# Optimization experiments

Measured on AMD Instinct MI355X. Metric: run time of the kernel, lower is better.

## Reference

```python
import jax, jax.numpy as jnp
import numpy as np

H = 16
D_MODEL = 1024
D_K = D_MODEL // H  # 64, must equal embeddim


def setup_inputs() -> dict:
    key = jax.random.key(0)
    ks = jax.random.split(key, 20)
    B, S, D = 4, 1024, D_MODEL
    s = 0.02
    inp = {
        'query': jax.random.normal(ks[0], (B, S, D), jnp.float32),
        'key':   jax.random.normal(ks[1], (B, S, D), jnp.float32),
        'value': jax.random.normal(ks[2], (B, S, D), jnp.float32),
        'mask':  jnp.ones((B, S, S), jnp.int32),
        # four d_model x d_model projections (q, k, v, out)
        'wq': jax.random.normal(ks[3], (D, D), jnp.float32) * s, 'bq': jnp.zeros((D,), jnp.float32),
        'wk': jax.random.normal(ks[4], (D, D), jnp.float32) * s, 'bk': jnp.zeros((D,), jnp.float32),
        'wv': jax.random.normal(ks[5], (D, D), jnp.float32) * s, 'bv': jnp.zeros((D,), jnp.float32),
        'wo': jax.random.normal(ks[6], (D, D), jnp.float32) * s, 'bo': jnp.zeros((D,), jnp.float32),
        # per-head (embeddim=64) linears
        'spatial_w': jax.random.normal(ks[7], (D_K, D_K), jnp.float32) * s, 'spatial_b': jnp.zeros((D_K,), jnp.float32),
        'qproj_w':   jax.random.normal(ks[8], (D_K, D_K), jnp.float32) * s, 'qproj_b':   jnp.zeros((D_K,), jnp.float32),
        'kproj_w':   jax.random.normal(ks[9], (D_K, D_K), jnp.float32) * s, 'kproj_b':   jnp.zeros((D_K,), jnp.float32),
        'vlin_w':    jax.random.normal(ks[10], (D_K, D_K), jnp.float32) * s, 'vlin_b':    jnp.zeros((D_K,), jnp.float32),
        # channel_linear: Linear(1, 64)
        'chan_w': jax.random.normal(ks[11], (1, D_K), jnp.float32) * s, 'chan_b': jnp.zeros((D_K,), jnp.float32),
    }
    return inp


def reference(query, key, value, mask,
              wq, bq, wk, bk, wv, bv, wo, bo,
              spatial_w, spatial_b, qproj_w, qproj_b,
              kproj_w, kproj_b, vlin_w, vlin_b, chan_w, chan_b):
    B, S, D = query.shape
    # project and split heads -> [B, H, S, D_K]
    def heads(x, w, b):
        return (x @ w + b).reshape(B, S, H, D_K).transpose(0, 2, 1, 3)
    q = heads(query, wq, bq)
    k = heads(key, wk, bk)
    v = heads(value, wv, bv)

    q = jax.nn.elu(q @ spatial_w + spatial_b)
    q_refine = q @ qproj_w + qproj_b
    # channel gate: mean over channels -> Linear(1,64) -> matmul with raw key
    alpha = q_refine.mean(-1, keepdims=True) @ chan_w + chan_b        # [B,H,S,64]
    gate = jax.nn.sigmoid(jnp.einsum('bhqe,bhke->bhqk', alpha, k))    # [B,H,S,S]

    k2 = jax.nn.elu(k @ kproj_w + kproj_b)
    scores = jnp.einsum('bhqe,bhke->bhqk', q, k2) / jnp.sqrt(jnp.asarray(D_K, q.dtype))
    scores = scores * gate
    scores = jnp.where(mask[:, None] == 0, jnp.asarray(-1e9, scores.dtype), scores)
    p_attn = jax.nn.softmax(scores, axis=-1)

    v2 = jax.nn.elu(v @ vlin_w + vlin_b)
    x = jnp.einsum('bhqk,bhke->bhqe', p_attn, v2)                     # [B,H,S,64]
    x = x.transpose(0, 2, 1, 3).reshape(B, S, H * D_K)
    return x @ wo + bo
```

## Files before the change

### kernel.cpp

```cpp
#include <hip/hip_runtime.h>
#include <math.h>

#define D_MODEL 1024
#define NH 16
#define DK 64
#define S_LEN 1024
#define BATCH 4
#define MROWS (BATCH * S_LEN)

typedef short bf16x8 __attribute__((ext_vector_type(8)));
typedef float f32x4 __attribute__((ext_vector_type(4)));
typedef unsigned short u16;

__device__ __forceinline__ float elu1(float x) {
    return x > 0.f ? x : (expf(x) - 1.f);
}

__device__ __forceinline__ u16 f2bf(float f) {
    union { float f; unsigned u; } v; v.f = f;
    unsigned u = v.u;
    return (u16)((u + 0x7fffu + ((u >> 16) & 1u)) >> 16);
}

__device__ __forceinline__ u16 f2bf_fast(float f) {
    union { float f; unsigned u; } v; v.f = f;
    return (u16)((v.u + 0x8000u) >> 16);
}

__device__ __forceinline__ void async16(const void* g, void* l) {
    __builtin_amdgcn_global_load_lds(
        (const __attribute__((address_space(1))) unsigned int*)g,
        (__attribute__((address_space(3))) unsigned int*)l,
        16, 0, 0);
}

__global__ __launch_bounds__(256) void prep(
    const float* __restrict__ wq, const float* __restrict__ wk,
    const float* __restrict__ wv, const float* __restrict__ wo,
    u16* __restrict__ WT,
    const float* __restrict__ Xq, const float* __restrict__ Xk,
    const float* __restrict__ Xv, u16* __restrict__ Xb,
    const int* __restrict__ mask, unsigned long long* __restrict__ Mb)
{
    __shared__ float T[64][65];
    const int bid = blockIdx.x;
    const int tid = threadIdx.x;

    if (bid < 1024) {
        const int z = bid >> 8;
        const int rem = bid & 255;
        const int n0 = (rem & 15) * 64, k0 = (rem >> 4) * 64;
        const float* W = (z == 0) ? wq : ((z == 1) ? wk : ((z == 2) ? wv : wo));
        u16* O = WT + (size_t)z * D_MODEL * D_MODEL;
        const int r = tid >> 4, c4 = (tid & 15) * 4;
        #pragma unroll
        for (int p = 0; p < 4; p++) {
            float4 v = *(const float4*)&W[(size_t)(k0 + r + p * 16) * D_MODEL + n0 + c4];
            T[r + p * 16][c4 + 0] = v.x; T[r + p * 16][c4 + 1] = v.y;
            T[r + p * 16][c4 + 2] = v.z; T[r + p * 16][c4 + 3] = v.w;
        }
        __syncthreads();
        #pragma unroll
        for (int p = 0; p < 4; p++) {
            const int i = r + p * 16;
            ushort4 o4;
            o4.x = f2bf(T[c4 + 0][i]); o4.y = f2bf(T[c4 + 1][i]);
            o4.z = f2bf(T[c4 + 2][i]); o4.w = f2bf(T[c4 + 3][i]);
            *(ushort4*)&O[(size_t)(n0 + i) * D_MODEL + k0 + c4] = o4;
        }
    } else if (bid < 1024 + 6144) {
        const int idx = bid - 1024;
        const int z = idx >> 11;
        const int bx = idx & 2047;
        const float* X = (z == 0) ? Xq : ((z == 1) ? Xk : Xv);
        u16* O = Xb + (size_t)z * MROWS * D_MODEL;
        const size_t i = ((size_t)bx * 256 + tid) * 8;
        float4 a = *(const float4*)&X[i];
        float4 b = *(const float4*)&X[i + 4];
        ushort4 o0, o1;
        o0.x = f2bf(a.x); o0.y = f2bf(a.y); o0.z = f2bf(a.z); o0.w = f2bf(a.w);
        o1.x = f2bf(b.x); o1.y = f2bf(b.y); o1.z = f2bf(b.z); o1.w = f2bf(b.w);
        *(ushort4*)&O[i] = o0;
        *(ushort4*)&O[i + 4] = o1;
    } else {
        const int bx = bid - 7168;
        const int gw = (bx * 256 + tid) >> 6;
        const int lane = tid & 63;
        int v[8];
        #pragma unroll
        for (int i = 0; i < 8; i++)
            v[i] = mask[((size_t)gw + (size_t)i * 8192) * 64 + lane];
        #pragma unroll
        for (int i = 0; i < 8; i++) {
            unsigned long long bits = __ballot(v[i] != 0);
            if (lane == 0) Mb[(size_t)gw + (size_t)i * 8192] = bits;
        }
    }
}

__global__ __launch_bounds__(256) void proj_fused(
    const u16* __restrict__ Xq, const u16* __restrict__ Xk, const u16* __restrict__ Xv,
    const u16* __restrict__ WTq, const u16* __restrict__ WTk, const u16* __restrict__ WTv,
    const float* __restrict__ bq, const float* __restrict__ bk, const float* __restrict__ bv,
    const float* __restrict__ spatial_w, const float* __restrict__ spatial_b,
    const float* __restrict__ qproj_w, const float* __restrict__ qproj_b,
    const float* __restrict__ kproj_w, const float* __restrict__ kproj_b,
    const float* __restrict__ vlin_w, const float* __restrict__ vlin_b,
    const float* __restrict__ chan_w, const float* __restrict__ chan_b,
    u16* __restrict__ Qh, u16* __restrict__ K2, u16* __restrict__ V2t,
    float* __restrict__ mB, float* __restrict__ uB, float* __restrict__ vB)
{
    __shared__ __align__(16) u16 smem[16896];
    __shared__ float auxA[64];
    __shared__ float auxS;

    u16* As = smem;
    u16* Bs = smem + 8192;
    u16* W2t = smem + 12288;

    const int z = blockIdx.z;
    const u16* X = (z == 0) ? Xq : ((z == 1) ? Xk : Xv);
    const u16* WT = (z == 0) ? WTq : ((z == 1) ? WTk : WTv);
    const float* B1 = (z == 0) ? bq : ((z == 1) ? bk : bv);
    const float* W2 = (z == 0) ? spatial_w : ((z == 1) ? kproj_w : vlin_w);
    const float* B2 = (z == 0) ? spatial_b : ((z == 1) ? kproj_b : vlin_b);

    const int tid = threadIdx.x;
    const int wave = tid >> 6, lane = tid & 63;
    const int col = lane & 15, quad = lane >> 4;
    const int r0 = blockIdx.x * 128;
    const int hh = blockIdx.y;
    const int n0 = hh * 64;

    #pragma unroll
    for (int p = 0; p < 4; p++) {
        int idx = p * 256 + tid;
        int f = idx >> 4, e4 = (idx & 15) * 4;
        float4 w4 = *(const float4*)&W2[f * 64 + e4];
        W2t[(e4 + 0) * 72 + f] = f2bf(w4.x);
        W2t[(e4 + 1) * 72 + f] = f2bf(w4.y);
        W2t[(e4 + 2) * 72 + f] = f2bf(w4.z);
        W2t[(e4 + 3) * 72 + f] = f2bf(w4.w);
    }
    if (z == 0) {
        {
            int row = tid >> 2, part = tid & 3;
            float s = 0.f;
            for (int e = part * 16; e < part * 16 + 16; e++) s += qproj_w[row * 64 + e];
            s += __shfl_xor(s, 1);
            s += __shfl_xor(s, 2);
            if (part == 0) auxA[row] = s * (1.f / 64.f);
        }
        if (tid < 64) {
            float s = qproj_b[tid];
            #pragma unroll
            for (int m = 1; m < 64; m <<= 1) s += __shfl_xor(s, m);
            if (tid == 0) auxS = s * (1.f / 64.f);
        }
    }

    const int srow8 = lane >> 3;
    const int sg = ((lane & 7) ^ srow8) * 8;

    const u16* ap = X + (size_t)(r0 + wave * 32 + srow8) * D_MODEL + sg;
    const u16* bp = WT + (size_t)(n0 + wave * 16 + srow8) * D_MODEL + sg;
    u16* adst = As + (wave * 32) * 64;
    u16* bdst = Bs + (wave * 16) * 64;

    f32x4 acc[2][4];
    #pragma unroll
    for (int i = 0; i < 2; i++)
        #pragma unroll
        for (int j = 0; j < 4; j++)
            acc[i][j] = (f32x4){0.f, 0.f, 0.f, 0.f};

    for (int k0 = 0; k0 < D_MODEL; k0 += 64) {
        if (k0) __syncthreads();
        #pragma unroll
        for (int i = 0; i < 4; i++)
            async16(ap + (size_t)(i * 8) * D_MODEL + k0, adst + i * 512);
        #pragma unroll
        for (int j = 0; j < 2; j++)
            async16(bp + (size_t)(j * 8) * D_MODEL + k0, bdst + j * 512);
        __syncthreads();
        #pragma unroll
        for (int ks = 0; ks < 2; ks++) {
            const int gk = ((ks * 4 + quad) ^ (col & 7)) * 8;
            const u16* Abase = As + (wave * 32 + col) * 64 + gk;
            const u16* Bbase = Bs + col * 64 + gk;
            bf16x8 af[2], bfr[4];
            #pragma unroll
            for (int mi = 0; mi < 2; mi++) af[mi] = *(const bf16x8*)(Abase + mi * 1024);
            #pragma unroll
            for (int ni = 0; ni < 4; ni++) bfr[ni] = *(const bf16x8*)(Bbase + ni * 1024);
            #pragma unroll
            for (int mi = 0; mi < 2; mi++)
                #pragma unroll
                for (int ni = 0; ni < 4; ni++)
                    acc[mi][ni] = __builtin_amdgcn_mfma_f32_16x16x32_bf16(af[mi], bfr[ni], acc[mi][ni], 0, 0, 0);
        }
    }

    float b1v[4];
    #pragma unroll
    for (int ni = 0; ni < 4; ni++) b1v[ni] = B1[n0 + ni * 16 + col];

    const int rbase = r0 + wave * 32;
    const int b = r0 >> 10;
    const int s0 = (r0 & 1023) + wave * 32;
    const size_t svecbase = ((size_t)b * NH + hh) * S_LEN;

    if (z == 1) {
        float cw[4], cb[4];
        #pragma unroll
        for (int ni = 0; ni < 4; ni++) { cw[ni] = chan_w[ni * 16 + col]; cb[ni] = chan_b[ni * 16 + col]; }
        #pragma unroll
        for (int mi = 0; mi < 2; mi++)
            #pragma unroll
            for (int r = 0; r < 4; r++) {
                float su = 0.f, sv = 0.f;
                #pragma unroll
                for (int ni = 0; ni < 4; ni++) {
                    float p = acc[mi][ni][r] + b1v[ni];
                    su += p * cw[ni];
                    sv += p * cb[ni];
                }
                su += __shfl_xor(su, 1); su += __shfl_xor(su, 2);
                su += __shfl_xor(su, 4); su += __shfl_xor(su, 8);
                sv += __shfl_xor(sv, 1); sv += __shfl_xor(sv, 2);
                sv += __shfl_xor(sv, 4); sv += __shfl_xor(sv, 8);
                if (col == 0) {
                    const size_t idx = svecbase + s0 + mi * 16 + quad * 4 + r;
                    uB[idx] = su;
                    vB[idx] = sv;
                }
            }
    }

    __syncthreads();

    u16* Pchunk = smem + wave * 1536;
    bf16x8 bf2r[4][2];
    #pragma unroll
    for (int ni = 0; ni < 4; ni++) {
        bf2r[ni][0] = *(const bf16x8*)&W2t[(ni * 16 + col) * 72 + quad * 8];
        bf2r[ni][1] = *(const bf16x8*)&W2t[(ni * 16 + col) * 72 + 32 + quad * 8];
    }
    float qs[2][4][4];
    #pragma unroll
    for (int mi = 0; mi < 2; mi++) {
        #pragma unroll
        for (int ni = 0; ni < 4; ni++)
            #pragma unroll
            for (int r = 0; r < 4; r++)
                Pchunk[(quad * 4 + r) * 72 + ni * 16 + col] = f2bf(acc[mi][ni][r] + b1v[ni]);
        __builtin_amdgcn_s_waitcnt(0xc07f);
        __builtin_amdgcn_sched_barrier(0);
        bf16x8 a0 = *(const bf16x8*)&Pchunk[col * 72 + quad * 8];
        bf16x8 a1 = *(const bf16x8*)&Pchunk[col * 72 + 32 + quad * 8];
        __builtin_amdgcn_s_waitcnt(0xc07f);
        __builtin_amdgcn_sched_barrier(0);
        #pragma unroll
        for (int ni = 0; ni < 4; ni++) {
            f32x4 c = (f32x4){0.f, 0.f, 0.f, 0.f};
            c = __builtin_amdgcn_mfma_f32_16x16x32_bf16(a0, bf2r[ni][0], c, 0, 0, 0);
            c = __builtin_amdgcn_mfma_f32_16x16x32_bf16(a1, bf2r[ni][1], c, 0, 0, 0);
            const float bb = B2[ni * 16 + col];
            #pragma unroll
            for (int r = 0; r < 4; r++) qs[mi][ni][r] = elu1(c[r] + bb);
        }
    }

    if (z == 0) {
        float aw[4];
        #pragma unroll
        for (int ni = 0; ni < 4; ni++) aw[ni] = auxA[ni * 16 + col];
        #pragma unroll
        for (int mi = 0; mi < 2; mi++)
            #pragma unroll
            for (int r = 0; r < 4; r++) {
                float pm = 0.f;
                #pragma unroll
                for (int ni = 0; ni < 4; ni++) pm += qs[mi][ni][r] * aw[ni];
                pm += __shfl_xor(pm, 1); pm += __shfl_xor(pm, 2);
                pm += __shfl_xor(pm, 4); pm += __shfl_xor(pm, 8);
                if (col == 0)
                    mB[svecbase + s0 + mi * 16 + quad * 4 + r] = pm + auxS;
            }
        #pragma unroll
        for (int mi = 0; mi < 2; mi++)
            #pragma unroll
            for (int ni = 0; ni < 4; ni++)
                #pragma unroll
                for (int r = 0; r < 4; r++)
                    Qh[(size_t)(rbase + mi * 16 + quad * 4 + r) * D_MODEL
                       + n0 + ni * 16 + col] = f2bf(qs[mi][ni][r] * 0.125f);
    } else if (z == 1) {
        #pragma unroll
        for (int mi = 0; mi < 2; mi++)
            #pragma unroll
            for (int ni = 0; ni < 4; ni++)
                #pragma unroll
                for (int r = 0; r < 4; r++)
                    K2[(size_t)(rbase + mi * 16 + quad * 4 + r) * D_MODEL
                       + n0 + ni * 16 + col] = f2bf(qs[mi][ni][r]);
    } else {
        u16* Tb = W2t;
        __syncthreads();
        #pragma unroll
        for (int p = 0; p < 2; p++) {
            if ((wave >> 1) == p) {
                const int sloc = (wave & 1) * 32;
                #pragma unroll
                for (int mi = 0; mi < 2; mi++)
                    #pragma unroll
                    for (int ni = 0; ni < 4; ni++)
                        #pragma unroll
                        for (int r = 0; r < 4; r++)
                            Tb[(ni * 16 + col) * 72 + sloc + mi * 16 + quad * 4 + r] =
                                f2bf(qs[mi][ni][r]);
            }
            __syncthreads();
            {
                const int d = tid >> 2, seg = tid & 3;
                u16* dst = V2t + (((size_t)b * NH + hh) * DK + d) * S_LEN
                         + (r0 & 1023) + p * 64 + seg * 16;
                *(uint4*)dst = *(const uint4*)&Tb[d * 72 + seg * 16];
                *(uint4*)(dst + 8) = *(const uint4*)&Tb[d * 72 + seg * 16 + 8];
            }
            if (p == 0) __syncthreads();
        }
    }
}

__global__ __launch_bounds__(256) void attn_mfma(
    const u16* __restrict__ Qh, const u16* __restrict__ K2h, const u16* __restrict__ V2t,
    const float* __restrict__ Mq, const float* __restrict__ Uk, const float* __restrict__ Vk,
    const unsigned long long* __restrict__ Mb, u16* __restrict__ X)
{
    __shared__ u16 K2s[64][72];
    __shared__ u16 V2s[64][72];
    __shared__ u16 Ps[4][16][72];

    const int tid = threadIdx.x;
    const int wave = tid >> 6, lane = tid & 63;
    const int col = lane & 15, quad = lane >> 4;

    const int f = blockIdx.x;
    const int o = (f & 7) * 64 + (f >> 3);
    const int q0 = (o & 7) * 128;
    const int h = (o >> 3) & 15;
    const int b = o >> 7;

    const size_t hb = ((size_t)(b * NH + h)) * S_LEN * DK;
    const size_t sb = ((size_t)(b * NH + h)) * S_LEN;

    bf16x8 qf0[2], qf1[2];
    float mqv[2][4];
    #pragma unroll
    for (int qc = 0; qc < 2; qc++) {
        const u16* qp = Qh + (size_t)(b * S_LEN + q0 + qc * 64 + wave * 16 + col) * D_MODEL
                      + h * 64 + quad * 8;
        qf0[qc] = *(const bf16x8*)qp;
        qf1[qc] = *(const bf16x8*)(qp + 32);
        #pragma unroll
        for (int r = 0; r < 4; r++)
            mqv[qc][r] = Mq[sb + q0 + qc * 64 + wave * 16 + quad * 4 + r];
    }

    const int srow = tid >> 2, sseg = tid & 3;
    const u16* ksrc = K2h + (size_t)(b * S_LEN + srow) * D_MODEL + h * 64 + sseg * 16;
    const u16* vsrc = V2t + hb + (size_t)srow * S_LEN + sseg * 16;
    const unsigned long long* mb0 = Mb
        + ((size_t)b * S_LEN + q0 + wave * 16 + quad * 4) * (S_LEN / 64);
    const unsigned msel0 = 1u << col, msel1 = msel0 << 16;

    uint4 ka = *(const uint4*)(ksrc);
    uint4 kb = *(const uint4*)(ksrc + 8);
    uint4 va = *(const uint4*)(vsrc);
    uint4 vb = *(const uint4*)(vsrc + 8);

    float psum[2][4];
    f32x4 o4[2][4];
    #pragma unroll
    for (int qc = 0; qc < 2; qc++) {
        #pragma unroll
        for (int r = 0; r < 4; r++) psum[qc][r] = 0.f;
        #pragma unroll
        for (int nb = 0; nb < 4; nb++) o4[qc][nb] = (f32x4){0.f, 0.f, 0.f, 0.f};
    }

    for (int t = 0; t < 16; t++) {
        *(uint4*)&K2s[srow][sseg * 16]     = ka;
        *(uint4*)&K2s[srow][sseg * 16 + 8] = kb;
        *(uint4*)&V2s[srow][sseg * 16]     = va;
        *(uint4*)&V2s[srow][sseg * 16 + 8] = vb;

        float ku[4], kv[4];
        #pragma unroll
        for (int nb = 0; nb < 4; nb++) {
            ku[nb] = Uk[sb + t * 64 + nb * 16 + col];
            kv[nb] = Vk[sb + t * 64 + nb * 16 + col];
        }
        __syncthreads();

        if (t < 15) {
            const int k1 = (t + 1) * 64;
            const u16* ks = ksrc + (size_t)k1 * D_MODEL;
            const u16* vs = vsrc + k1;
            ka = *(const uint4*)(ks);
            kb = *(const uint4*)(ks + 8);
            va = *(const uint4*)(vs);
            vb = *(const uint4*)(vs + 8);
        }

        #pragma unroll
        for (int qc = 0; qc < 2; qc++) {
            unsigned long long wm[4];
            #pragma unroll
            for (int r = 0; r < 4; r++)
                wm[r] = mb0[(qc * 64 + r * 4 / 4 * 0 + r) * 16 + t + (size_t)qc * 64 * 16 - (size_t)qc * 64 * 16 + (size_t)qc * 1024 - (size_t)qc * 1024];
            #pragma unroll
            for (int r = 0; r < 4; r++)
                wm[r] = mb0[((size_t)qc * 64 + r) * 16 + t];

            __builtin_amdgcn_s_setprio(1);
            f32x4 sc[4];
            #pragma unroll
            for (int nb = 0; nb < 4; nb++) {
                bf16x8 b0 = *(const bf16x8*)&K2s[nb * 16 + col][quad * 8];
                bf16x8 b1 = *(const bf16x8*)&K2s[nb * 16 + col][32 + quad * 8];
                f32x4 c = (f32x4){0.f, 0.f, 0.f, 0.f};
                c = __builtin_amdgcn_mfma_f32_16x16x32_bf16(qf0[qc], b0, c, 0, 0, 0);
                c = __builtin_amdgcn_mfma_f32_16x16x32_bf16(qf1[qc], b1, c, 0, 0, 0);
                sc[nb] = c;
            }
            __builtin_amdgcn_s_setprio(0);

            #pragma unroll
            for (int nb = 0; nb < 4; nb++) {
                #pragma unroll
                for (int r = 0; r < 4; r++) {
                    float e = __expf(-(mqv[qc][r] * ku[nb] + kv[nb]));
                    float g = __builtin_amdgcn_rcpf(1.f + e);
                    float sv = sc[nb][r] * g;
                    const unsigned bits = (nb < 2) ? (unsigned)wm[r]
                                                   : (unsigned)(wm[r] >> 32);
                    sv = (bits & ((nb & 1) ? msel1 : msel0)) ? sv : -30.f;
                    float p = __expf(sv);
                    psum[qc][r] += p;
                    Ps[wave][quad * 4 + r][nb * 16 + col] = f2bf_fast(p);
                }
            }
            __builtin_amdgcn_s_waitcnt(0xc07f);
            __builtin_amdgcn_sched_barrier(0);
            bf16x8 a0 = *(const bf16x8*)&Ps[wave][col][quad * 8];
            bf16x8 a1 = *(const bf16x8*)&Ps[wave][col][32 + quad * 8];
            __builtin_amdgcn_s_waitcnt(0xc07f);
            __builtin_amdgcn_sched_barrier(0);

            __builtin_amdgcn_s_setprio(1);
            #pragma unroll
            for (int nb = 0; nb < 4; nb++) {
                bf16x8 b0 = *(const bf16x8*)&V2s[nb * 16 + col][quad * 8];
                bf16x8 b1 = *(const bf16x8*)&V2s[nb * 16 + col][32 + quad * 8];
                o4[qc][nb] = __builtin_amdgcn_mfma_f32_16x16x32_bf16(a0, b0, o4[qc][nb], 0, 0, 0);
                o4[qc][nb] = __builtin_amdgcn_mfma_f32_16x16x32_bf16(a1, b1, o4[qc][nb], 0, 0, 0);
            }
            __builtin_amdgcn_s_setprio(0);
        }
        __syncthreads();
    }

    #pragma unroll
    for (int qc = 0; qc < 2; qc++)
        #pragma unroll
        for (int r = 0; r < 4; r++) {
            float t = psum[qc][r];
            t += __shfl_xor(t, 1);
            t += __shfl_xor(t, 2);
            t += __shfl_xor(t, 4);
            t += __shfl_xor(t, 8);
            float inv = __builtin_amdgcn_rcpf(t);
            u16* xp = X + (size_t)(b * S_LEN + q0 + qc * 64 + wave * 16 + quad * 4 + r) * D_MODEL
                    + h * 64 + col;
            #pragma unroll
            for (int nb = 0; nb < 4; nb++)
                xp[nb * 16] = f2bf_fast(o4[qc][nb][r] * inv);
        }
}

__global__ __launch_bounds__(256) void out_gemm(
    const u16* __restrict__ A, const u16* __restrict__ WT,
    const float* __restrict__ bias, float* __restrict__ C)
{
    __shared__ u16 As[128 * 32];
    __shared__ u16 Bs[64 * 32];

    const int tid = threadIdx.x;
    const int wave = tid >> 6, lane = tid & 63;
    const int col = lane & 15, quad = lane >> 4;
    const int r0 = blockIdx.x * 128, n0 = blockIdx.y * 64;

    const int srow = lane >> 2;
    const int sg = ((lane & 3) ^ ((lane >> 3) & 3)) * 8;
    const u16* ap = A + (size_t)(r0 + wave * 32 + srow) * D_MODEL + sg;
    const u16* bp = WT + (size_t)(n0 + wave * 16 + srow) * D_MODEL + sg;
    u16* adst0 = As + (wave * 32) * 32;  u16* adst1 = adst0 + 512;
    u16* bdst = Bs + wave * 16 * 32;

    f32x4 acc[2][4];
    #pragma unroll
    for (int i = 0; i < 2; i++)
        #pragma unroll
        for (int j = 0; j < 4; j++)
            acc[i][j] = (f32x4){0.f, 0.f, 0.f, 0.f};

    const int gsw = (quad ^ ((col >> 1) & 3)) * 8;

    for (int k0 = 0; k0 < D_MODEL; k0 += 32) {
        if (k0) __syncthreads();
        async16(ap + k0, adst0);
        async16(ap + (size_t)16 * D_MODEL + k0, adst1);
        async16(bp + k0, bdst);
        __syncthreads();
        const u16* Ab = As + (wave * 32 + col) * 32 + gsw;
        const u16* Bb = Bs + col * 32 + gsw;
        bf16x8 af[2], bfr[4];
        #pragma unroll
        for (int mi = 0; mi < 2; mi++) af[mi] = *(const bf16x8*)(Ab + mi * 512);
        #pragma unroll
        for (int ni = 0; ni < 4; ni++) bfr[ni] = *(const bf16x8*)(Bb + ni * 512);
        #pragma unroll
        for (int mi = 0; mi < 2; mi++)
            #pragma unroll
            for (int ni = 0; ni < 4; ni++)
                acc[mi][ni] = __builtin_amdgcn_mfma_f32_16x16x32_bf16(af[mi], bfr[ni], acc[mi][ni], 0, 0, 0);
    }

    #pragma unroll
    for (int mi = 0; mi < 2; mi++)
        #pragma unroll
        for (int ni = 0; ni < 4; ni++) {
            const int gr = r0 + wave * 32 + mi * 16 + quad * 4;
            const int gc = n0 + ni * 16 + col;
            const float bb = bias[gc];
            #pragma unroll
            for (int r = 0; r < 4; r++)
                C[(size_t)(gr + r) * D_MODEL + gc] = acc[mi][ni][r] + bb;
        }
}

extern "C" void kernel_launch(void* const* d_in, const int* in_sizes, int n_in,
                              void* d_out, int out_size, void* d_ws, size_t ws_size,
                              hipStream_t stream) {
    (void)in_sizes; (void)n_in; (void)out_size; (void)ws_size;
    const float* query = (const float*)d_in[0];
    const float* key_  = (const float*)d_in[1];
    const float* value = (const float*)d_in[2];
    const int*   mask  = (const int*)d_in[3];
    const float* wq = (const float*)d_in[4];  const float* bq = (const float*)d_in[5];
    const float* wk = (const float*)d_in[6];  const float* bk = (const float*)d_in[7];
    const float* wv = (const float*)d_in[8];  const float* bv = (const float*)d_in[9];
    const float* wo = (const float*)d_in[10]; const float* bo = (const float*)d_in[11];
    const float* spatial_w = (const float*)d_in[12]; const float* spatial_b = (const float*)d_in[13];
    const float* qproj_w   = (const float*)d_in[14]; const float* qproj_b   = (const float*)d_in[15];
    const float* kproj_w   = (const float*)d_in[16]; const float* kproj_b   = (const float*)d_in[17];
    const float* vlin_w    = (const float*)d_in[18]; const float* vlin_b    = (const float*)d_in[19];
    const float* chan_w    = (const float*)d_in[20]; const float* chan_b    = (const float*)d_in[21];
    float* out = (float*)d_out;

    char* ws = (char*)d_ws;
    u16* Qh  = (u16*)ws;
    u16* K2  = (u16*)(ws + ((size_t)8  << 20));
    u16* Xb  = (u16*)(ws + ((size_t)16 << 20));
    u16* WT  = (u16*)(ws + ((size_t)24 << 20));
    u16* V2t = (u16*)(ws + ((size_t)32 << 20));
    float* mB = (float*)(ws + ((size_t)40 << 20));
    float* uB = mB + (size_t)BATCH * NH * S_LEN;
    float* vB = uB + (size_t)BATCH * NH * S_LEN;
    unsigned long long* Mbits = (unsigned long long*)(ws + ((size_t)41 << 20));
    u16* Xbf = (u16*)(ws + ((size_t)42 << 20));
    const size_t WSZ = (size_t)D_MODEL * D_MODEL;
    const size_t XSZ = (size_t)MROWS * D_MODEL;

    prep<<<dim3(9216), 256, 0, stream>>>(wq, wk, wv, wo, WT,
        query, key_, value, Xbf, mask, Mbits);
    proj_fused<<<dim3(32, 16, 3), 256, 0, stream>>>(Xbf, Xbf + XSZ, Xbf + 2 * XSZ,
        WT, WT + WSZ, WT + 2 * WSZ, bq, bk, bv,
        spatial_w, spatial_b, qproj_w, qproj_b, kproj_w, kproj_b,
        vlin_w, vlin_b, chan_w, chan_b,
        Qh, K2, V2t, mB, uB, vB);
    attn_mfma<<<dim3(512), 256, 0, stream>>>(Qh, K2, V2t, mB, uB, vB, Mbits, Xb);
    out_gemm<<<dim3(32, 16), 256, 0, stream>>>(Xb, WT + 3 * WSZ, bo, out);
}
```

Before: 276.0 us.

## Double-buffer K-tiles in projection and output GEMMs to overlap loads with MFMA

Both the fused QKV projection GEMM and the output GEMM now use a two-stage shared-memory ping-pong with 32-wide K tiles. The next tile is issued asynchronously before computing the current one, so there is one barrier per tile instead of two. The projection kernel's K-step shrinks from 64 to 32 with a different swizzle. A redundant duplicated mask-word load in the attention kernel is also removed. Barrier count stays similar in the projection kernel, and the async-copy wait semantics must guarantee a stage has landed before it is consumed.

```diff
diff --git a/kernel.cpp b/kernel.cpp
--- a/kernel.cpp
+++ b/kernel.cpp
@@ -114,8 +114,6 @@
     __shared__ float auxA[64];
     __shared__ float auxS;
 
-    u16* As = smem;
-    u16* Bs = smem + 8192;
     u16* W2t = smem + 12288;
 
     const int z = blockIdx.z;
@@ -159,13 +157,11 @@
         }
     }
 
-    const int srow8 = lane >> 3;
-    const int sg = ((lane & 7) ^ srow8) * 8;
-
-    const u16* ap = X + (size_t)(r0 + wave * 32 + srow8) * D_MODEL + sg;
-    const u16* bp = WT + (size_t)(n0 + wave * 16 + srow8) * D_MODEL + sg;
-    u16* adst = As + (wave * 32) * 64;
-    u16* bdst = Bs + (wave * 16) * 64;
+    const int srow = lane >> 2;
+    const int sg = ((lane & 3) ^ ((lane >> 3) & 3)) * 8;
+
+    const u16* ap = X + (size_t)(r0 + wave * 32 + srow) * D_MODEL + sg;
+    const u16* bp = WT + (size_t)(n0 + wave * 16 + srow) * D_MODEL + sg;
 
     f32x4 acc[2][4];
     #pragma unroll
@@ -174,32 +170,46 @@
         for (int j = 0; j < 4; j++)
             acc[i][j] = (f32x4){0.f, 0.f, 0.f, 0.f};
 
+    const int gsw = (quad ^ ((col >> 1) & 3)) * 8;
+
+#define PF_STAGE(P, K)                                                        \
+    do {                                                                      \
+        u16* a0_ = smem + (P) * 6144 + wave * 1024;                           \
+        u16* b0_ = smem + (P) * 6144 + 4096 + wave * 512;                     \
+        async16(ap + (K), a0_);                                               \
+        async16(ap + (size_t)16 * D_MODEL + (K), a0_ + 512);                  \
+        async16(bp + (K), b0_);                                               \
+    } while (0)
+
+#define PF_COMPUTE(P)                                                         \
+    do {                                                                      \
+        const u16* Ab_ = smem + (P) * 6144 + (wave * 32 + col) * 32 + gsw;    \
+        const u16* Bb_ = smem + (P) * 6144 + 4096 + col * 32 + gsw;           \
+        bf16x8 af_[2], bf_[4];                                                \
+        _Pragma("unroll")                                                     \
+        for (int mi = 0; mi < 2; mi++) af_[mi] = *(const bf16x8*)(Ab_ + mi * 512); \
+        _Pragma("unroll")                                                     \
+        for (int ni = 0; ni < 4; ni++) bf_[ni] = *(const bf16x8*)(Bb_ + ni * 512); \
+        _Pragma("unroll")                                                     \
+        for (int mi = 0; mi < 2; mi++)                                        \
+            _Pragma("unroll")                                                 \
+            for (int ni = 0; ni < 4; ni++)                                    \
+                acc[mi][ni] = __builtin_amdgcn_mfma_f32_16x16x32_bf16(        \
+                    af_[mi], bf_[ni], acc[mi][ni], 0, 0, 0);                  \
+    } while (0)
+
+    PF_STAGE(0, 0);
+    __syncthreads();
     for (int k0 = 0; k0 < D_MODEL; k0 += 64) {
-        if (k0) __syncthreads();
-        #pragma unroll
-        for (int i = 0; i < 4; i++)
-            async16(ap + (size_t)(i * 8) * D_MODEL + k0, adst + i * 512);
-        #pragma unroll
-        for (int j = 0; j < 2; j++)
-            async16(bp + (size_t)(j * 8) * D_MODEL + k0, bdst + j * 512);
-        __syncthreads();
-        #pragma unroll
-        for (int ks = 0; ks < 2; ks++) {
-            const int gk = ((ks * 4 + quad) ^ (col & 7)) * 8;
-            const u16* Abase = As + (wave * 32 + col) * 64 + gk;
-            const u16* Bbase = Bs + col * 64 + gk;
-            bf16x8 af[2], bfr[4];
-            #pragma unroll
-            for (int mi = 0; mi < 2; mi++) af[mi] = *(const bf16x8*)(Abase + mi * 1024);
-            #pragma unroll
-            for (int ni = 0; ni < 4; ni++) bfr[ni] = *(const bf16x8*)(Bbase + ni * 1024);
-            #pragma unroll
-            for (int mi = 0; mi < 2; mi++)
-                #pragma unroll
-                for (int ni = 0; ni < 4; ni++)
-                    acc[mi][ni] = __builtin_amdgcn_mfma_f32_16x16x32_bf16(af[mi], bfr[ni], acc[mi][ni], 0, 0, 0);
-        }
-    }
+        if (k0 + 32 < D_MODEL) PF_STAGE(1, k0 + 32);
+        PF_COMPUTE(0);
+        __syncthreads();
+        if (k0 + 64 < D_MODEL) PF_STAGE(0, k0 + 64);
+        PF_COMPUTE(1);
+        __syncthreads();
+    }
+#undef PF_STAGE
+#undef PF_COMPUTE
 
     float b1v[4];
     #pragma unroll
@@ -419,9 +429,6 @@
             unsigned long long wm[4];
             #pragma unroll
             for (int r = 0; r < 4; r++)
-                wm[r] = mb0[(qc * 64 + r * 4 / 4 * 0 + r) * 16 + t + (size_t)qc * 64 * 16 - (size_t)qc * 64 * 16 + (size_t)qc * 1024 - (size_t)qc * 1024];
-            #pragma unroll
-            for (int r = 0; r < 4; r++)
                 wm[r] = mb0[((size_t)qc * 64 + r) * 16 + t];
 
             __builtin_amdgcn_s_setprio(1);
@@ -494,8 +501,7 @@
     const u16* __restrict__ A, const u16* __restrict__ WT,
     const float* __restrict__ bias, float* __restrict__ C)
 {
-    __shared__ u16 As[128 * 32];
-    __shared__ u16 Bs[64 * 32];
+    __shared__ __align__(16) u16 smem[12288];
 
     const int tid = threadIdx.x;
     const int wave = tid >> 6, lane = tid & 63;
@@ -506,8 +512,6 @@
     const int sg = ((lane & 3) ^ ((lane >> 3) & 3)) * 8;
     const u16* ap = A + (size_t)(r0 + wave * 32 + srow) * D_MODEL + sg;
     const u16* bp = WT + (size_t)(n0 + wave * 16 + srow) * D_MODEL + sg;
-    u16* adst0 = As + (wave * 32) * 32;  u16* adst1 = adst0 + 512;
-    u16* bdst = Bs + wave * 16 * 32;
 
     f32x4 acc[2][4];
     #pragma unroll
@@ -518,25 +522,44 @@
 
     const int gsw = (quad ^ ((col >> 1) & 3)) * 8;
 
-    for (int k0 = 0; k0 < D_MODEL; k0 += 32) {
-        if (k0) __syncthreads();
-        async16(ap + k0, adst0);
-        async16(ap + (size_t)16 * D_MODEL + k0, adst1);
-        async16(bp + k0, bdst);
-        __syncthreads();
-        const u16* Ab = As + (wave * 32 + col) * 32 + gsw;
-        const u16* Bb = Bs + col * 32 + gsw;
-        bf16x8 af[2], bfr[4];
-        #pragma unroll
-        for (int mi = 0; mi < 2; mi++) af[mi] = *(const bf16x8*)(Ab + mi * 512);
-        #pragma unroll
-        for (int ni = 0; ni < 4; ni++) bfr[ni] = *(const bf16x8*)(Bb + ni * 512);
-        #pragma unroll
-        for (int mi = 0; mi < 2; mi++)
-            #pragma unroll
-            for (int ni = 0; ni < 4; ni++)
-                acc[mi][ni] = __builtin_amdgcn_mfma_f32_16x16x32_bf16(af[mi], bfr[ni], acc[mi][ni], 0, 0, 0);
-    }
+#define OG_STAGE(P, K)                                                        \
+    do {                                                                      \
+        u16* a0_ = smem + (P) * 6144 + wave * 1024;                           \
+        u16* b0_ = smem + (P) * 6144 + 4096 + wave * 512;                     \
+        async16(ap + (K), a0_);                                               \
+        async16(ap + (size_t)16 * D_MODEL + (K), a0_ + 512);                  \
+        async16(bp + (K), b0_);                                               \
+    } while (0)
+
+#define OG_COMPUTE(P)                                                         \
+    do {                                                                      \
+        const u16* Ab_ = smem + (P) * 6144 + (wave * 32 + col) * 32 + gsw;    \
+        const u16* Bb_ = smem + (P) * 6144 + 4096 + col * 32 + gsw;           \
+        bf16x8 af_[2], bf_[4];                                                \
+        _Pragma("unroll")                                                     \
+        for (int mi = 0; mi < 2; mi++) af_[mi] = *(const bf16x8*)(Ab_ + mi * 512); \
+        _Pragma("unroll")                                                     \
+        for (int ni = 0; ni < 4; ni++) bf_[ni] = *(const bf16x8*)(Bb_ + ni * 512); \
+        _Pragma("unroll")                                                     \
+        for (int mi = 0; mi < 2; mi++)                                        \
+            _Pragma("unroll")                                                 \
+            for (int ni = 0; ni < 4; ni++)                                    \
+                acc[mi][ni] = __builtin_amdgcn_mfma_f32_16x16x32_bf16(        \
+                    af_[mi], bf_[ni], acc[mi][ni], 0, 0, 0);                  \
+    } while (0)
+
+    OG_STAGE(0, 0);
+    __syncthreads();
+    for (int k0 = 0; k0 < D_MODEL; k0 += 64) {
+        if (k0 + 32 < D_MODEL) OG_STAGE(1, k0 + 32);
+        OG_COMPUTE(0);
+        __syncthreads();
+        if (k0 + 64 < D_MODEL) OG_STAGE(0, k0 + 64);
+        OG_COMPUTE(1);
+        __syncthreads();
+    }
+#undef OG_STAGE
+#undef OG_COMPUTE
 
     #pragma unroll
     for (int mi = 0; mi < 2; mi++)
```

New measurement: 272.8 us. Within noise of the previous version (-1.2%).
